# Performance work log

Measured on AMD Instinct MI355X. Metric: run time of the kernel, lower is better.

## Reference

```python
import jax, jax.numpy as jnp
import numpy as np

N_QUBITS = 10
N_LAYERS = 3


def _apply_1q(state, gate, q, batched):
    # state: (B,) + (2,)*n ; gate: (2,2) or (B,2,2)
    s = jnp.moveaxis(state, q + 1, -1)
    shp = s.shape
    s = s.reshape(shp[0], -1, 2)
    eq = 'bij,brj->bri' if batched else 'ij,brj->bri'
    s = jnp.einsum(eq, gate, s).reshape(shp)
    return jnp.moveaxis(s, -1, q + 1)


def _apply_cnot(state, c, t):
    s = jnp.moveaxis(state, (c + 1, t + 1), (-2, -1))
    s = s.at[..., 1, :].set(s[..., 1, ::-1])  # flip target where control==1
    return jnp.moveaxis(s, (-2, -1), (c + 1, t + 1))


def _rot_gate(phi, theta, omega):
    # PennyLane Rot(phi,theta,omega) = RZ(omega) @ RY(theta) @ RZ(phi)
    ch = jnp.cos(theta * 0.5).astype(jnp.complex64)
    sh = jnp.sin(theta * 0.5).astype(jnp.complex64)
    m00 = jnp.exp(-1j * (phi + omega) * 0.5) * ch
    m01 = -jnp.exp(1j * (phi - omega) * 0.5) * sh
    m10 = jnp.exp(-1j * (phi - omega) * 0.5) * sh
    m11 = jnp.exp(1j * (phi + omega) * 0.5) * ch
    return jnp.stack([jnp.stack([m00, m01]), jnp.stack([m10, m11])])


def _circuit(x, weights):
    B = x.shape[0]
    n = N_QUBITS
    state = jnp.zeros((B,) + (2,) * n, jnp.complex64)
    state = state.at[(slice(None),) + (0,) * n].set(1.0)  # |0...0>
    c = jnp.cos(x * 0.5)  # (B, n)
    s = jnp.sin(x * 0.5)
    for l in range(N_LAYERS):
        # AngleEmbedding: RY(x_q) on each wire (batched gates)
        for q in range(n):
            g = jnp.stack([jnp.stack([c[:, q], -s[:, q]], -1),
                           jnp.stack([s[:, q], c[:, q]], -1)], -2).astype(jnp.complex64)
            state = _apply_1q(state, g, q, True)
        # StronglyEntanglingLayers, single sub-layer: Rot on each wire
        for q in range(n):
            g = _rot_gate(weights[l, q, 0], weights[l, q, 1], weights[l, q, 2])
            state = _apply_1q(state, g, q, False)
        # ring of CNOTs with range r=1
        for q in range(n):
            state = _apply_cnot(state, q, (q + 1) % n)
    probs = jnp.abs(state) ** 2  # (B,) + (2,)*n, real
    outs = []
    for q in range(n):
        axes = tuple(a for a in range(1, n + 1) if a != q + 1)
        m = probs.sum(axis=axes)  # (B, 2)
        outs.append(m[:, 0] - m[:, 1])  # <Z_q>
    return jnp.stack(outs, axis=1).astype(jnp.float32)


def setup_inputs() -> dict:
    key = jax.random.key(0)
    k1, k2 = jax.random.split(key)
    x = jax.random.normal(k1, (4096, N_QUBITS), dtype=jnp.float32)
    weights = jax.random.uniform(k2, (N_LAYERS, N_QUBITS, 3), dtype=jnp.float32,
                                 minval=-np.pi, maxval=np.pi)
    return {"x": x, "weights": weights}


def reference(x, weights):
    return _circuit(x, weights)
```

## Files before the change

### kernel.cpp

```cpp
#include <hip/hip_runtime.h>

#define NQ 10
#define NL 3

__device__ __forceinline__ float2 cxmul(float2 c, float2 v) {
    return make_float2(fmaf(c.x, v.x, -c.y * v.y), fmaf(c.x, v.y, c.y * v.x));
}
__device__ __forceinline__ float2 cxmad(float2 c, float2 v, float2 acc) {
    acc.x = fmaf(c.x, v.x, fmaf(-c.y, v.y, acc.x));
    acc.y = fmaf(c.x, v.y, fmaf( c.y, v.x, acc.y));
    return acc;
}
__device__ __forceinline__ float2 shxor2(float2 v, int m) {
    return make_float2(__shfl_xor(v.x, m, 64), __shfl_xor(v.y, m, 64));
}

template<int MASK, int RMASK>
__device__ __forceinline__ void apply_gate(float2 (&a)[16],
        float2 m00, float2 m01, float2 m10, float2 m11, int lane)
{
    constexpr int LM = (MASK >> 4) & 63;
    constexpr int JM = MASK & 15;
    constexpr int RH = (RMASK >> 4) & 63;
    constexpr int RL = RMASK & 15;

    const int lp = (RH != 0) ? (__popc(lane & RH) & 1) : 0;
    const float2 cA0 = lp ? m11 : m00, cB0 = lp ? m10 : m01;
    const float2 cA1 = lp ? m00 : m11, cB1 = lp ? m01 : m10;

    if constexpr (JM == 0) {
        #pragma unroll
        for (int j = 0; j < 16; ++j) {
            float2 other = shxor2(a[j], LM);
            const int sp = __builtin_popcount(j & RL) & 1;
            const float2 cA = sp ? cA1 : cA0, cB = sp ? cB1 : cB0;
            a[j] = cxmad(cB, other, cxmul(cA, a[j]));
        }
    } else {
        constexpr int HB = 1 << (31 - __builtin_clz((unsigned)JM));
        #pragma unroll
        for (int j = 0; j < 16; ++j) {
            if (j & HB) continue;
            const int k = j ^ JM;
            const float2 aj = a[j], ak = a[k];
            float2 oj, ok;
            if constexpr (LM != 0) { oj = shxor2(ak, LM); ok = shxor2(aj, LM); }
            else                   { oj = ak;             ok = aj;             }
            const int spj = __builtin_popcount(j & RL) & 1;
            const int spk = __builtin_popcount(k & RL) & 1;
            const float2 cAj = spj ? cA1 : cA0, cBj = spj ? cB1 : cB0;
            const float2 cAk = spk ? cA1 : cA0, cBk = spk ? cB1 : cB0;
            a[j] = cxmad(cBj, oj, cxmul(cAj, aj));
            a[k] = cxmad(cBk, ok, cxmul(cAk, ak));
        }
    }
}

__global__ __launch_bounds__(256, 4)
void qnn_kernel(const float* __restrict__ x, const float* __restrict__ w,
                float* __restrict__ out)
{
    __shared__ float4 rotL[NL * NQ][2];

    const int t    = threadIdx.x;
    const int lane = t & 63;
    const int b    = blockIdx.x * 4 + (t >> 6);

    if (t < NL * NQ) {
        const float* wp = w + t * 3;
        float phi = wp[0], th = wp[1], om = wp[2];
        float ct = cosf(th * 0.5f), st = sinf(th * 0.5f);
        float ap = (phi + om) * 0.5f, am = (phi - om) * 0.5f;
        float cap = cosf(ap), sap = sinf(ap);
        float cam = cosf(am), sam = sinf(am);
        rotL[t][0] = make_float4(cap * ct, -sap * ct, -cam * st, -sam * st);
        rotL[t][1] = make_float4(cam * st, -sam * st,  cap * ct,  sap * ct);
    }
    __syncthreads();

    float myc = 0.f, mys = 0.f;
    if (lane < NQ) {
        float xv = x[b * NQ + lane] * 0.5f;
        myc = __cosf(xv);
        mys = __sinf(xv);
    }

    float2 a[16];
    #pragma unroll
    for (int j = 0; j < 16; ++j) a[j] = make_float2(0.f, 0.f);
    if (lane == 0) a[0].x = 1.f;

#define GATE(IDX, Q, MASK, RMASK) do {                                        \
        const float4 r0 = rotL[IDX][0];                                       \
        const float4 r1 = rotL[IDX][1];                                       \
        const float cq = __shfl(myc, Q, 64);                                  \
        const float sq = __shfl(mys, Q, 64);                                  \
        const float2 g00 = make_float2(fmaf(r0.x, cq,  r0.z * sq),            \
                                       fmaf(r0.y, cq,  r0.w * sq));           \
        const float2 g01 = make_float2(fmaf(r0.z, cq, -r0.x * sq),            \
                                       fmaf(r0.w, cq, -r0.y * sq));           \
        const float2 g10 = make_float2(fmaf(r1.x, cq,  r1.z * sq),            \
                                       fmaf(r1.y, cq,  r1.w * sq));           \
        const float2 g11 = make_float2(fmaf(r1.z, cq, -r1.x * sq),            \
                                       fmaf(r1.w, cq, -r1.y * sq));           \
        apply_gate<MASK, RMASK>(a, g00, g01, g10, g11, lane);                 \
    } while (0)

    GATE( 0, 0, 0x001, 0x001);  GATE( 1, 1, 0x002, 0x002);
    GATE( 2, 2, 0x004, 0x004);  GATE( 3, 3, 0x008, 0x008);
    GATE( 4, 4, 0x010, 0x010);  GATE( 5, 5, 0x020, 0x020);
    GATE( 6, 6, 0x040, 0x040);  GATE( 7, 7, 0x080, 0x080);
    GATE( 8, 8, 0x100, 0x100);  GATE( 9, 9, 0x200, 0x200);
    GATE(10, 0, 0x003, 0x3FE);  GATE(11, 1, 0x006, 0x003);
    GATE(12, 2, 0x00C, 0x007);  GATE(13, 3, 0x018, 0x00F);
    GATE(14, 4, 0x030, 0x01F);  GATE(15, 5, 0x060, 0x03F);
    GATE(16, 6, 0x0C0, 0x07F);  GATE(17, 7, 0x180, 0x0FF);
    GATE(18, 8, 0x300, 0x1FF);  GATE(19, 9, 0x203, 0x3FF);
    GATE(20, 0, 0x005, 0x2AB);  GATE(21, 1, 0x00A, 0x3FD);
    GATE(22, 2, 0x014, 0x3FA);  GATE(23, 3, 0x028, 0x3F5);
    GATE(24, 4, 0x050, 0x3EA);  GATE(25, 5, 0x0A0, 0x3D5);
    GATE(26, 6, 0x140, 0x3AA);  GATE(27, 7, 0x280, 0x355);
    GATE(28, 8, 0x103, 0x2AA);  GATE(29, 9, 0x206, 0x155);
#undef GATE

    float P[16];
    #pragma unroll
    for (int j = 0; j < 16; ++j)
        P[j] = fmaf(a[j].x, a[j].x, a[j].y * a[j].y);

    float vout = 0.f;
#define MEAS(Q, RMASK) do {                                                   \
        constexpr int RH = ((RMASK) >> 4) & 63, RL = (RMASK) & 15;            \
        float v = 0.f;                                                        \
        _Pragma("unroll")                                                     \
        for (int j = 0; j < 16; ++j)                                          \
            v += (__builtin_popcount(j & RL) & 1) ? -P[j] : P[j];             \
        if (__popc(lane & RH) & 1) v = -v;                                    \
        v += __shfl_xor(v, 32, 64); v += __shfl_xor(v, 16, 64);               \
        v += __shfl_xor(v,  8, 64); v += __shfl_xor(v,  4, 64);               \
        v += __shfl_xor(v,  2, 64); v += __shfl_xor(v,  1, 64);               \
        if (lane == Q) vout = v;                                              \
    } while (0)

    MEAS(0, 0x0CD); MEAS(1, 0x156); MEAS(2, 0x2AC); MEAS(3, 0x159);
    MEAS(4, 0x2B3); MEAS(5, 0x166); MEAS(6, 0x2CC); MEAS(7, 0x199);
    MEAS(8, 0x333); MEAS(9, 0x266);
#undef MEAS

    if (lane < NQ) out[b * NQ + lane] = vout;
}

extern "C" void kernel_launch(void* const* d_in, const int* in_sizes, int n_in,
                              void* d_out, int out_size, void* d_ws, size_t ws_size,
                              hipStream_t stream) {
    const float* x = (const float*)d_in[0];
    const float* w = (const float*)d_in[1];
    float* out = (float*)d_out;
    const int B = in_sizes[0] / NQ;
    qnn_kernel<<<B / 4, 256, 0, stream>>>(x, w, out);
}
```

Before: 92.91 us.

## Build first-layer product state analytically and use packed FMA, DPP and swizzle shuffles

The first layer acts on |0...0> with single-qubit gates only, so its state is now built directly as a tensor product of per-qubit columns, which removes ten gate applications. Gate application now uses v_pk_mul/v_pk_fma inline asm with op_sel to pick the gate coefficient by parity. Cross-lane exchanges use DPP, ds_swizzle or bpermute instead of generic shuffles. Measurement applies a Walsh-Hadamard transform over the 16 register probabilities, so each qubit needs only one parity-sign lookup before its reduction. The costs are complex inline asm that depends on exact op_sel semantics, and per-lane scalar loads of x.

```diff
diff --git a/kernel.cpp b/kernel.cpp
--- a/kernel.cpp
+++ b/kernel.cpp
@@ -3,56 +3,125 @@
 #define NQ 10
 #define NL 3
 
-__device__ __forceinline__ float2 cxmul(float2 c, float2 v) {
-    return make_float2(fmaf(c.x, v.x, -c.y * v.y), fmaf(c.x, v.y, c.y * v.x));
-}
-__device__ __forceinline__ float2 cxmad(float2 c, float2 v, float2 acc) {
-    acc.x = fmaf(c.x, v.x, fmaf(-c.y, v.y, acc.x));
-    acc.y = fmaf(c.x, v.y, fmaf( c.y, v.x, acc.y));
-    return acc;
-}
-__device__ __forceinline__ float2 shxor2(float2 v, int m) {
-    return make_float2(__shfl_xor(v.x, m, 64), __shfl_xor(v.y, m, 64));
+typedef float v2f __attribute__((ext_vector_type(2)));
+
+__device__ __forceinline__ int   f2i(float v) { union { float f; int i; } u; u.f = v; return u.i; }
+__device__ __forceinline__ float i2f(int v)   { union { int i; float f; } u; u.i = v; return u.f; }
+
+__device__ __forceinline__ v2f cmul(v2f a, v2f b) {
+    return (v2f){ fmaf(a.x, b.x, -a.y * b.y), fmaf(a.x, b.y, a.y * b.x) };
+}
+
+template<int SP> __device__ __forceinline__ v2f pk_mul_sel(v2f a, v2f K) {
+    v2f d;
+    if constexpr (SP == 0)
+        asm("v_pk_mul_f32 %0, %1, %2 op_sel:[0,0] op_sel_hi:[1,0]" : "=v"(d) : "v"(a), "v"(K));
+    else
+        asm("v_pk_mul_f32 %0, %1, %2 op_sel:[0,1] op_sel_hi:[1,1]" : "=v"(d) : "v"(a), "v"(K));
+    return d;
+}
+template<int SP> __device__ __forceinline__ v2f pk_fma_sel(v2f a, v2f K, v2f c) {
+    v2f d;
+    if constexpr (SP == 0)
+        asm("v_pk_fma_f32 %0, %1, %2, %3 op_sel:[0,0,0] op_sel_hi:[1,0,1]"
+            : "=v"(d) : "v"(a), "v"(K), "v"(c));
+    else
+        asm("v_pk_fma_f32 %0, %1, %2, %3 op_sel:[0,1,0] op_sel_hi:[1,1,1]"
+            : "=v"(d) : "v"(a), "v"(K), "v"(c));
+    return d;
+}
+template<int SP> __device__ __forceinline__ v2f pk_fma_i_sel(v2f a, v2f K, v2f c) {
+    v2f d;
+    if constexpr (SP == 0)
+        asm("v_pk_fma_f32 %0, %1, %2, %3 op_sel:[1,0,0] op_sel_hi:[0,0,1] neg_lo:[1,0,0]"
+            : "=v"(d) : "v"(a), "v"(K), "v"(c));
+    else
+        asm("v_pk_fma_f32 %0, %1, %2, %3 op_sel:[1,1,0] op_sel_hi:[0,1,1] neg_lo:[1,0,0]"
+            : "=v"(d) : "v"(a), "v"(K), "v"(c));
+    return d;
+}
+
+template<int LM>
+__device__ __forceinline__ v2f xlane(v2f v, int baddr) {
+    int x = f2i(v.x), y = f2i(v.y);
+    if constexpr (LM == 1) {
+        x = __builtin_amdgcn_mov_dpp(x, 177, 0xF, 0xF, false);
+        y = __builtin_amdgcn_mov_dpp(y, 177, 0xF, 0xF, false);
+    } else if constexpr (LM == 2) {
+        x = __builtin_amdgcn_mov_dpp(x, 78, 0xF, 0xF, false);
+        y = __builtin_amdgcn_mov_dpp(y, 78, 0xF, 0xF, false);
+    } else if constexpr (LM == 3) {
+        x = __builtin_amdgcn_mov_dpp(x, 27, 0xF, 0xF, false);
+        y = __builtin_amdgcn_mov_dpp(y, 27, 0xF, 0xF, false);
+    } else if constexpr (LM < 32) {
+        constexpr int off = (LM << 10) | 0x1F;
+        x = __builtin_amdgcn_ds_swizzle(x, off);
+        y = __builtin_amdgcn_ds_swizzle(y, off);
+    } else {
+        x = __builtin_amdgcn_ds_bpermute(baddr, x);
+        y = __builtin_amdgcn_ds_bpermute(baddr, y);
+    }
+    return (v2f){ i2f(x), i2f(y) };
 }
 
 template<int MASK, int RMASK>
-__device__ __forceinline__ void apply_gate(float2 (&a)[16],
-        float2 m00, float2 m01, float2 m10, float2 m11, int lane)
+__device__ __forceinline__ void apply_gate(v2f (&a)[16], float4 r0, float4 r1,
+                                           float cq, float sq, int lane)
 {
     constexpr int LM = (MASK >> 4) & 63;
     constexpr int JM = MASK & 15;
     constexpr int RH = (RMASK >> 4) & 63;
     constexpr int RL = RMASK & 15;
 
+    const float g00r = fmaf(r0.x, cq,  r0.z * sq), g00i = fmaf(r0.y, cq,  r0.w * sq);
+    const float g01r = fmaf(r0.z, cq, -r0.x * sq), g01i = fmaf(r0.w, cq, -r0.y * sq);
+    const float g10r = fmaf(r1.x, cq,  r1.z * sq), g10i = fmaf(r1.y, cq,  r1.w * sq);
+    const float g11r = fmaf(r1.z, cq, -r1.x * sq), g11i = fmaf(r1.w, cq, -r1.y * sq);
+
     const int lp = (RH != 0) ? (__popc(lane & RH) & 1) : 0;
-    const float2 cA0 = lp ? m11 : m00, cB0 = lp ? m10 : m01;
-    const float2 cA1 = lp ? m00 : m11, cB1 = lp ? m01 : m10;
+    const v2f KAr = lp ? (v2f){g11r, g00r} : (v2f){g00r, g11r};
+    const v2f KAi = lp ? (v2f){g11i, g00i} : (v2f){g00i, g11i};
+    const v2f KBr = lp ? (v2f){g10r, g01r} : (v2f){g01r, g10r};
+    const v2f KBi = lp ? (v2f){g10i, g01i} : (v2f){g01i, g10i};
+
+    const int baddr = ((lane ^ LM) << 2);
 
     if constexpr (JM == 0) {
-        #pragma unroll
-        for (int j = 0; j < 16; ++j) {
-            float2 other = shxor2(a[j], LM);
-            const int sp = __builtin_popcount(j & RL) & 1;
-            const float2 cA = sp ? cA1 : cA0, cB = sp ? cB1 : cB0;
-            a[j] = cxmad(cB, other, cxmul(cA, a[j]));
-        }
+#define QNN_X(J)                                                              \
+        { constexpr int SP_ = __builtin_popcount((J) & RL) & 1;               \
+          v2f o_ = xlane<LM>(a[J], baddr);                                    \
+          v2f t_ = pk_mul_sel<SP_>(a[J], KAr);                                \
+          t_ = pk_fma_i_sel<SP_>(a[J], KAi, t_);                              \
+          t_ = pk_fma_sel<SP_>(o_, KBr, t_);                                  \
+          t_ = pk_fma_i_sel<SP_>(o_, KBi, t_);                                \
+          a[J] = t_; }
+        QNN_X(0) QNN_X(1) QNN_X(2) QNN_X(3) QNN_X(4) QNN_X(5) QNN_X(6) QNN_X(7)
+        QNN_X(8) QNN_X(9) QNN_X(10) QNN_X(11) QNN_X(12) QNN_X(13) QNN_X(14) QNN_X(15)
+#undef QNN_X
     } else {
         constexpr int HB = 1 << (31 - __builtin_clz((unsigned)JM));
-        #pragma unroll
-        for (int j = 0; j < 16; ++j) {
-            if (j & HB) continue;
-            const int k = j ^ JM;
-            const float2 aj = a[j], ak = a[k];
-            float2 oj, ok;
-            if constexpr (LM != 0) { oj = shxor2(ak, LM); ok = shxor2(aj, LM); }
-            else                   { oj = ak;             ok = aj;             }
-            const int spj = __builtin_popcount(j & RL) & 1;
-            const int spk = __builtin_popcount(k & RL) & 1;
-            const float2 cAj = spj ? cA1 : cA0, cBj = spj ? cB1 : cB0;
-            const float2 cAk = spk ? cA1 : cA0, cBk = spk ? cB1 : cB0;
-            a[j] = cxmad(cBj, oj, cxmul(cAj, aj));
-            a[k] = cxmad(cBk, ok, cxmul(cAk, ak));
+#define QNN_P(J)                                                              \
+        if constexpr (((J) & HB) == 0) {                                      \
+            constexpr int K_  = (J) ^ JM;                                     \
+            constexpr int SPJ = __builtin_popcount((J) & RL) & 1;             \
+            constexpr int SPK = __builtin_popcount(K_  & RL) & 1;             \
+            v2f aj_ = a[J], ak_ = a[K_];                                      \
+            v2f oj_, ok_;                                                     \
+            if constexpr (LM != 0) { oj_ = xlane<LM>(ak_, baddr);             \
+                                     ok_ = xlane<LM>(aj_, baddr); }           \
+            else                   { oj_ = ak_; ok_ = aj_; }                  \
+            { v2f t_ = pk_mul_sel<SPJ>(aj_, KAr);                             \
+              t_ = pk_fma_i_sel<SPJ>(aj_, KAi, t_);                           \
+              t_ = pk_fma_sel<SPJ>(oj_, KBr, t_);                             \
+              t_ = pk_fma_i_sel<SPJ>(oj_, KBi, t_);  a[J]  = t_; }            \
+            { v2f t_ = pk_mul_sel<SPK>(ak_, KAr);                             \
+              t_ = pk_fma_i_sel<SPK>(ak_, KAi, t_);                           \
+              t_ = pk_fma_sel<SPK>(ok_, KBr, t_);                             \
+              t_ = pk_fma_i_sel<SPK>(ok_, KBi, t_);  a[K_] = t_; }            \
         }
+        QNN_P(0) QNN_P(1) QNN_P(2) QNN_P(3) QNN_P(4) QNN_P(5) QNN_P(6) QNN_P(7)
+        QNN_P(8) QNN_P(9) QNN_P(10) QNN_P(11) QNN_P(12) QNN_P(13) QNN_P(14) QNN_P(15)
+#undef QNN_P
     }
 }
 
@@ -78,73 +147,88 @@
     }
     __syncthreads();
 
-    float myc = 0.f, mys = 0.f;
-    if (lane < NQ) {
-        float xv = x[b * NQ + lane] * 0.5f;
-        myc = __cosf(xv);
-        mys = __sinf(xv);
-    }
-
-    float2 a[16];
-    #pragma unroll
-    for (int j = 0; j < 16; ++j) a[j] = make_float2(0.f, 0.f);
-    if (lane == 0) a[0].x = 1.f;
-
-#define GATE(IDX, Q, MASK, RMASK) do {                                        \
-        const float4 r0 = rotL[IDX][0];                                       \
-        const float4 r1 = rotL[IDX][1];                                       \
-        const float cq = __shfl(myc, Q, 64);                                  \
-        const float sq = __shfl(mys, Q, 64);                                  \
-        const float2 g00 = make_float2(fmaf(r0.x, cq,  r0.z * sq),            \
-                                       fmaf(r0.y, cq,  r0.w * sq));           \
-        const float2 g01 = make_float2(fmaf(r0.z, cq, -r0.x * sq),            \
-                                       fmaf(r0.w, cq, -r0.y * sq));           \
-        const float2 g10 = make_float2(fmaf(r1.x, cq,  r1.z * sq),            \
-                                       fmaf(r1.y, cq,  r1.w * sq));           \
-        const float2 g11 = make_float2(fmaf(r1.z, cq, -r1.x * sq),            \
-                                       fmaf(r1.w, cq, -r1.y * sq));           \
-        apply_gate<MASK, RMASK>(a, g00, g01, g10, g11, lane);                 \
-    } while (0)
-
-    GATE( 0, 0, 0x001, 0x001);  GATE( 1, 1, 0x002, 0x002);
-    GATE( 2, 2, 0x004, 0x004);  GATE( 3, 3, 0x008, 0x008);
-    GATE( 4, 4, 0x010, 0x010);  GATE( 5, 5, 0x020, 0x020);
-    GATE( 6, 6, 0x040, 0x040);  GATE( 7, 7, 0x080, 0x080);
-    GATE( 8, 8, 0x100, 0x100);  GATE( 9, 9, 0x200, 0x200);
-    GATE(10, 0, 0x003, 0x3FE);  GATE(11, 1, 0x006, 0x003);
-    GATE(12, 2, 0x00C, 0x007);  GATE(13, 3, 0x018, 0x00F);
-    GATE(14, 4, 0x030, 0x01F);  GATE(15, 5, 0x060, 0x03F);
-    GATE(16, 6, 0x0C0, 0x07F);  GATE(17, 7, 0x180, 0x0FF);
-    GATE(18, 8, 0x300, 0x1FF);  GATE(19, 9, 0x203, 0x3FF);
-    GATE(20, 0, 0x005, 0x2AB);  GATE(21, 1, 0x00A, 0x3FD);
-    GATE(22, 2, 0x014, 0x3FA);  GATE(23, 3, 0x028, 0x3F5);
-    GATE(24, 4, 0x050, 0x3EA);  GATE(25, 5, 0x0A0, 0x3D5);
-    GATE(26, 6, 0x140, 0x3AA);  GATE(27, 7, 0x280, 0x355);
-    GATE(28, 8, 0x103, 0x2AA);  GATE(29, 9, 0x206, 0x155);
+    const float* xb = x + (size_t)__builtin_amdgcn_readfirstlane(b * NQ);
+    float c_[NQ], s_[NQ];
+    #pragma unroll
+    for (int q = 0; q < NQ; ++q) {
+        float xv = xb[q] * 0.5f;
+        c_[q] = __cosf(xv);
+        s_[q] = __sinf(xv);
+    }
+
+    v2f c0[4], c1[4];
+    v2f Ln = {1.f, 0.f};
+    #pragma unroll
+    for (int q = 0; q < NQ; ++q) {
+        float4 r0 = rotL[q][0], r1 = rotL[q][1];
+        float cq = c_[q], sq = s_[q];
+        v2f g0 = { fmaf(r0.x, cq, r0.z * sq), fmaf(r0.y, cq, r0.w * sq) };
+        v2f g1 = { fmaf(r1.x, cq, r1.z * sq), fmaf(r1.y, cq, r1.w * sq) };
+        if (q < 4) { c0[q] = g0; c1[q] = g1; }
+        else {
+            v2f gg = ((lane >> (q - 4)) & 1) ? g1 : g0;
+            Ln = (q == 4) ? gg : cmul(Ln, gg);
+        }
+    }
+    v2f S01[4], SH[4];
+    #pragma unroll
+    for (int j = 0; j < 4; ++j)
+        S01[j] = cmul((j & 1) ? c1[0] : c0[0], (j & 2) ? c1[1] : c0[1]);
+    #pragma unroll
+    for (int h = 0; h < 4; ++h)
+        SH[h] = cmul(cmul((h & 1) ? c1[2] : c0[2], (h & 2) ? c1[3] : c0[3]), Ln);
+    v2f a[16];
+    #pragma unroll
+    for (int j = 0; j < 16; ++j)
+        a[j] = cmul(S01[j & 3], SH[j >> 2]);
+
+#define GATE(IDX, Q, MASK, RMASK) \
+    apply_gate<MASK, RMASK>(a, rotL[IDX][0], rotL[IDX][1], c_[Q], s_[Q], lane);
+    GATE(10, 0, 0x003, 0x3FE)  GATE(11, 1, 0x006, 0x003)
+    GATE(12, 2, 0x00C, 0x007)  GATE(13, 3, 0x018, 0x00F)
+    GATE(14, 4, 0x030, 0x01F)  GATE(15, 5, 0x060, 0x03F)
+    GATE(16, 6, 0x0C0, 0x07F)  GATE(17, 7, 0x180, 0x0FF)
+    GATE(18, 8, 0x300, 0x1FF)  GATE(19, 9, 0x203, 0x3FF)
+    GATE(20, 0, 0x005, 0x2AB)  GATE(21, 1, 0x00A, 0x3FD)
+    GATE(22, 2, 0x014, 0x3FA)  GATE(23, 3, 0x028, 0x3F5)
+    GATE(24, 4, 0x050, 0x3EA)  GATE(25, 5, 0x0A0, 0x3D5)
+    GATE(26, 6, 0x140, 0x3AA)  GATE(27, 7, 0x280, 0x355)
+    GATE(28, 8, 0x103, 0x2AA)  GATE(29, 9, 0x206, 0x155)
 #undef GATE
 
     float P[16];
     #pragma unroll
     for (int j = 0; j < 16; ++j)
         P[j] = fmaf(a[j].x, a[j].x, a[j].y * a[j].y);
-
+    #pragma unroll
+    for (int bit = 0; bit < 4; ++bit) {
+        #pragma unroll
+        for (int j = 0; j < 16; ++j)
+            if (!(j & (1 << bit))) {
+                int k = j | (1 << bit);
+                float u = P[j], v = P[k];
+                P[j] = u + v;
+                P[k] = u - v;
+            }
+    }
+
+    const int bp32 = ((lane ^ 32) << 2);
     float vout = 0.f;
-#define MEAS(Q, RMASK) do {                                                   \
-        constexpr int RH = ((RMASK) >> 4) & 63, RL = (RMASK) & 15;            \
-        float v = 0.f;                                                        \
-        _Pragma("unroll")                                                     \
-        for (int j = 0; j < 16; ++j)                                          \
-            v += (__builtin_popcount(j & RL) & 1) ? -P[j] : P[j];             \
-        if (__popc(lane & RH) & 1) v = -v;                                    \
-        v += __shfl_xor(v, 32, 64); v += __shfl_xor(v, 16, 64);               \
-        v += __shfl_xor(v,  8, 64); v += __shfl_xor(v,  4, 64);               \
-        v += __shfl_xor(v,  2, 64); v += __shfl_xor(v,  1, 64);               \
-        if (lane == Q) vout = v;                                              \
-    } while (0)
-
-    MEAS(0, 0x0CD); MEAS(1, 0x156); MEAS(2, 0x2AC); MEAS(3, 0x159);
-    MEAS(4, 0x2B3); MEAS(5, 0x166); MEAS(6, 0x2CC); MEAS(7, 0x199);
-    MEAS(8, 0x333); MEAS(9, 0x266);
+#define MEAS(Q, RM)                                                           \
+    { constexpr int RH_ = ((RM) >> 4) & 63;                                   \
+      constexpr int RL_ = (RM) & 15;                                          \
+      float v = P[RL_];                                                       \
+      if (__popc(lane & RH_) & 1) v = -v;                                     \
+      v += i2f(__builtin_amdgcn_mov_dpp(f2i(v), 177, 0xF, 0xF, false));       \
+      v += i2f(__builtin_amdgcn_mov_dpp(f2i(v), 78, 0xF, 0xF, false));        \
+      v += i2f(__builtin_amdgcn_ds_swizzle(f2i(v), (4 << 10) | 0x1F));        \
+      v += i2f(__builtin_amdgcn_ds_swizzle(f2i(v), (8 << 10) | 0x1F));        \
+      v += i2f(__builtin_amdgcn_ds_swizzle(f2i(v), (16 << 10) | 0x1F));       \
+      v += i2f(__builtin_amdgcn_ds_bpermute(bp32, f2i(v)));                   \
+      if (lane == (Q)) vout = v; }
+    MEAS(0, 0x0CD) MEAS(1, 0x156) MEAS(2, 0x2AC) MEAS(3, 0x159)
+    MEAS(4, 0x2B3) MEAS(5, 0x166) MEAS(6, 0x2CC) MEAS(7, 0x199)
+    MEAS(8, 0x333) MEAS(9, 0x266)
 #undef MEAS
 
     if (lane < NQ) out[b * NQ + lane] = vout;
```

Result: faster. 79.17 us (-14.8%).
